# Optimization experiments

Hardware: AMD Instinct MI355X
Metric: run time of the kernel (lower is better)

## Reference

```python
import jax, jax.numpy as jnp
import numpy as np

EPS = 1e-5

def setup_inputs() -> dict:
    key = jax.random.key(0)
    k1, k2, k3 = jax.random.split(key, 3)
    x = jax.random.normal(k1, (16, 256, 32, 32), dtype=jnp.float32)
    embed = jax.random.normal(k2, (8192, 256), dtype=jnp.float32)
    cluster_size = jax.random.uniform(k3, (8192,), dtype=jnp.float32)
    return {"x": x, "embed": embed, "cluster_size": cluster_size}

def reference(x, embed, cluster_size):
    # x: (b, c, h, w) -> (b, h*w, c); project_in is Identity (codebook_dim == dim, heads=1)
    b, c, h, w = x.shape
    xt = jnp.transpose(x, (0, 2, 3, 1)).reshape(b, h * w, c)   # (b, n, d)
    flat = xt.reshape(-1, c)                                    # (N, d)
    d2 = (jnp.sum(flat * flat, axis=1, keepdims=True)
          - 2.0 * flat @ embed.T
          + jnp.sum(embed * embed, axis=1))                     # (N, K)
    embed_ind_flat = jnp.argmin(d2, axis=-1)                    # (N,) temperature==0 -> argmax of -d2
    quantize = embed[embed_ind_flat].reshape(b, h * w, c)       # gather codebook rows
    embed_ind = embed_ind_flat.reshape(b, h * w)
    # perplexity over (unnormalized) EMA cluster sizes, as in the torch code
    probs = cluster_size
    perplexity = jnp.exp(-jnp.sum(probs * jnp.log(probs + EPS)))
    # eval-mode commitment loss (weight_loss=True, commitment_weight=1.0)
    commit_loss = jnp.mean((quantize - xt) ** 2)
    return quantize, embed_ind, perplexity, commit_loss
```

## Files before the change

kernel.cpp:

```cpp
#include <hip/hip_runtime.h>
#include <hip/hip_bf16.h>
#include <math.h>

typedef _Float16 f16x8 __attribute__((ext_vector_type(8)));
typedef float f32x4 __attribute__((ext_vector_type(4)));

#define N_TOK 16384
#define D 256
#define K 8192

#define Q_OFF 0
#define IND_OFF 4194304
#define PERP_OFF 4210688
#define COMMIT_OFF 4210689

#define WS_CAND   0u
#define WS_E2     1048576u
#define WS_DSUM   1081344u
#define WS_EH     1114112u
#define WS_XH     5308416u
#define WS_XT     13697024u
#define WS_NEED   30474240u

__device__ __forceinline__ unsigned int ford(float f) {
    unsigned int u = __float_as_uint(f);
    return (u & 0x80000000u) ? ~u : (u | 0x80000000u);
}
__device__ __forceinline__ unsigned short f2h(float f) {
    _Float16 h = (_Float16)f;
    return *(unsigned short*)&h;
}
__device__ __forceinline__ void gload16(const void* g, void* l) {
    __builtin_amdgcn_global_load_lds(
        (const __attribute__((address_space(1))) unsigned int*)g,
        (__attribute__((address_space(3))) unsigned int*)l, 16, 0, 0);
}


__global__ void vq_convert_x(const float* __restrict__ x, float* __restrict__ xt,
                             unsigned short* __restrict__ xh) {
    __shared__ float t[64][65];
    const int tid = threadIdx.x;
    const int p0 = blockIdx.x * 64, c0 = blockIdx.y * 64, b = blockIdx.z;
    const int q = tid & 15, h = tid >> 4;
    #pragma unroll
    for (int r = 0; r < 4; ++r) {
        const int cl = r * 16 + h;
        const float4 v = *(const float4*)(x + (((size_t)(b * 256 + c0 + cl)) << 10) + p0 + q * 4);
        t[cl][q * 4 + 0] = v.x; t[cl][q * 4 + 1] = v.y;
        t[cl][q * 4 + 2] = v.z; t[cl][q * 4 + 3] = v.w;
    }
    __syncthreads();
    #pragma unroll
    for (int r = 0; r < 4; ++r) {
        const int nl = r * 16 + h;
        const int n = (b << 10) + p0 + nl;
        const int c = c0 + q * 4;
        float4 vf; ushort4 vh;
        vf.x = t[q * 4 + 0][nl]; vf.y = t[q * 4 + 1][nl];
        vf.z = t[q * 4 + 2][nl]; vf.w = t[q * 4 + 3][nl];
        vh.x = f2h(vf.x); vh.y = f2h(vf.y); vh.z = f2h(vf.z); vh.w = f2h(vf.w);
        *(float4*)(xt + ((size_t)n << 8) + c) = vf;
        *(ushort4*)(xh + ((size_t)n << 8) + c) = vh;
    }
}

__global__ void vq_prep_e(const float* __restrict__ e, unsigned short* __restrict__ eh,
                          float* __restrict__ e2, double* __restrict__ dsum) {
    if (blockIdx.x == 0 && threadIdx.x == 0) *dsum = 0.0;
    const int wave = threadIdx.x >> 6, lane = threadIdx.x & 63;
    const int c = blockIdx.x * 4 + wave;
    const float4 v = *(const float4*)(e + (size_t)c * D + lane * 4);
    ushort4 vh;
    vh.x = f2h(v.x); vh.y = f2h(v.y); vh.z = f2h(v.z); vh.w = f2h(v.w);
    *(ushort4*)(eh + (size_t)c * D + lane * 4) = vh;
    float s = v.x * v.x + v.y * v.y + v.z * v.z + v.w * v.w;
    #pragma unroll
    for (int off = 32; off > 0; off >>= 1) s += __shfl_down(s, off, 64);
    if (lane == 0) e2[c] = s;
}

__global__ __launch_bounds__(256)
__attribute__((amdgpu_waves_per_eu(2, 2)))
void vq_mfma_kernel(
    const unsigned short* __restrict__ xh, const unsigned short* __restrict__ eh,
    const float* __restrict__ e2, unsigned int* __restrict__ cand) {
    __shared__ __align__(16) unsigned short Bs[2][64 * 256];
    __shared__ float e2s[1024];

    const int tid = threadIdx.x;
    const int lane = tid & 63, wid = tid >> 6;
    const int l15 = lane & 15, lg = lane >> 4;
    const int split = blockIdx.y;
    const int m0 = blockIdx.x * 256;
    const int c0s = split * 1024;
    const int rw = m0 + wid * 64;

    *(float4*)&e2s[tid * 4] = *(const float4*)(e2 + c0s + tid * 4);

    f16x8 a[4][8];
    #pragma unroll
    for (int mf = 0; mf < 4; ++mf) {
        const unsigned short* ap = xh + (((size_t)(rw + mf * 16 + l15)) << 8) + lg * 8;
        #pragma unroll
        for (int t = 0; t < 8; ++t)
            a[mf][t] = *(const f16x8*)(ap + t * 32);
    }
    #pragma unroll
    for (int mf = 0; mf < 4; ++mf)
        #pragma unroll
        for (int t = 0; t < 8; ++t)
            asm volatile("" : "+v"(*(f32x4*)&a[mf][t]));

    __syncthreads();

    const int r0 = tid >> 5, cc = tid & 31;
    const unsigned short* ebase =
        eh + (((size_t)(c0s + r0)) << 8) + ((cc ^ r0) << 3);
    char* wdst = (char*)Bs + tid * 16;
    auto stage = [&](int t, int bo) {
        const unsigned short* p = ebase + t * 16384;
        #pragma unroll
        for (int i = 0; i < 8; ++i)
            gload16(p + i * 2048, wdst + bo + i * 4096);
    };

    const char* rbase = (const char*)Bs + l15 * 512;
    int ko[8];
    #pragma unroll
    for (int pr = 0; pr < 8; ++pr) ko[pr] = (((4 * pr + lg) ^ (l15 & 7)) << 4);

    float d1[16], d2[16];
    unsigned int ipk[16];
    #pragma unroll
    for (int r = 0; r < 16; ++r) { d1[r] = INFINITY; d2[r] = INFINITY; ipk[r] = 0; }

    stage(0, 0);

    #pragma unroll 2
    for (int t = 0; t < 16; ++t) {
        asm volatile("s_waitcnt vmcnt(0)" ::: "memory");
        __builtin_amdgcn_s_barrier();
        if (t < 15) stage(t + 1, ((t + 1) & 1) * 32768);

        const int BUF = (t & 1) * 32768;
        #pragma unroll
        for (int s2 = 0; s2 < 2; ++s2) {
            const int sb = BUF + s2 * 16384;
            const float e2v0 = e2s[t * 64 + s2 * 32 + l15];
            const float e2v1 = e2s[t * 64 + s2 * 32 + 16 + l15];
            f32x4 acc[4][2];
            #pragma unroll
            for (int mf = 0; mf < 4; ++mf) {
                f32x4 z = {0.f, 0.f, 0.f, 0.f};
                acc[mf][0] = z; acc[mf][1] = z;
            }
            f16x8 b0a = *(const f16x8*)(rbase + ko[0] + sb);
            f16x8 b1a = *(const f16x8*)(rbase + ko[0] + sb + 8192);
            #pragma unroll
            for (int pr = 0; pr < 8; ++pr) {
                f16x8 b0n, b1n;
                if (pr < 7) {
                    b0n = *(const f16x8*)(rbase + ko[pr + 1] + sb);
                    b1n = *(const f16x8*)(rbase + ko[pr + 1] + sb + 8192);
                }
                #pragma unroll
                for (int mf = 0; mf < 4; ++mf) {
                    acc[mf][0] = __builtin_amdgcn_mfma_f32_16x16x32_f16(
                        a[mf][pr], b0a, acc[mf][0], 0, 0, 0);
                    acc[mf][1] = __builtin_amdgcn_mfma_f32_16x16x32_f16(
                        a[mf][pr], b1a, acc[mf][1], 0, 0, 0);
                }
                b0a = b0n; b1a = b1n;
            }
            const unsigned int cl0 = (unsigned int)(t * 64 + s2 * 32 + l15);
            #pragma unroll
            for (int mf = 0; mf < 4; ++mf) {
                #pragma unroll
                for (int reg = 0; reg < 4; ++reg) {
                    const int rr = mf * 4 + reg;
                    const float sc0 = fmaf(-2.0f, acc[mf][0][reg], e2v0);
                    const float sc1 = fmaf(-2.0f, acc[mf][1][reg], e2v1);
                    if (fminf(sc0, sc1) < d2[rr]) {
                        {
                            const bool lt1 = sc0 < d1[rr], lt2 = sc0 < d2[rr];
                            const unsigned int ii = ipk[rr];
                            const unsigned int nif = (ii << 16) | cl0;
                            const unsigned int nis = (ii & 0xFFFFu) | (cl0 << 16);
                            d2[rr] = lt1 ? d1[rr] : (lt2 ? sc0 : d2[rr]);
                            ipk[rr] = lt1 ? nif : (lt2 ? nis : ii);
                            d1[rr] = lt1 ? sc0 : d1[rr];
                        }
                        {
                            const unsigned int cl1 = cl0 + 16;
                            const bool lt1 = sc1 < d1[rr], lt2 = sc1 < d2[rr];
                            const unsigned int ii = ipk[rr];
                            const unsigned int nif = (ii << 16) | cl1;
                            const unsigned int nis = (ii & 0xFFFFu) | (cl1 << 16);
                            d2[rr] = lt1 ? d1[rr] : (lt2 ? sc1 : d2[rr]);
                            ipk[rr] = lt1 ? nif : (lt2 ? nis : ii);
                            d1[rr] = lt1 ? sc1 : d1[rr];
                        }
                    }
                }
            }
        }
    }

    unsigned long long p1[16], p2[16];
    #pragma unroll
    for (int r = 0; r < 16; ++r) {
        p1[r] = (((unsigned long long)ford(d1[r])) << 32) |
                (unsigned int)(c0s + (ipk[r] & 0xFFFFu));
        p2[r] = (((unsigned long long)ford(d2[r])) << 32) |
                (unsigned int)(c0s + (ipk[r] >> 16));
    }
    #pragma unroll
    for (int st = 1; st < 16; st <<= 1) {
        #pragma unroll
        for (int r = 0; r < 16; ++r) {
            const unsigned long long q1 = __shfl_xor(p1[r], st, 64);
            const unsigned long long q2 = __shfl_xor(p2[r], st, 64);
            const unsigned long long n1 = p1[r] < q1 ? p1[r] : q1;
            const unsigned long long hi = p1[r] < q1 ? q1 : p1[r];
            const unsigned long long l2 = p2[r] < q2 ? p2[r] : q2;
            p1[r] = n1;
            p2[r] = hi < l2 ? hi : l2;
        }
    }
    if (l15 == 0) {
        #pragma unroll
        for (int mf = 0; mf < 4; ++mf)
            #pragma unroll
            for (int reg = 0; reg < 4; ++reg) {
                const int n = rw + mf * 16 + lg * 4 + reg;
                unsigned int* cp = cand + (((size_t)n) << 4) + split * 2;
                cp[0] = (unsigned int)p1[mf * 4 + reg];
                cp[1] = (unsigned int)p2[mf * 4 + reg];
            }
    }
}

__global__ void vq_rescore_finalize(const float* __restrict__ xt, const float* __restrict__ embed,
                                    const float* __restrict__ e2,
                                    const unsigned int* __restrict__ cand,
                                    float* __restrict__ out, double* __restrict__ dsum) {
    __shared__ double red[4];
    const int tid = threadIdx.x, wid = tid >> 6, lane = tid & 63;
    double wsum = 0.0;
    #pragma unroll 1
    for (int it = 0; it < 8; ++it) {
        const int n = blockIdx.x * 32 + it * 4 + wid;
        const float4 xv = *(const float4*)(xt + (((size_t)n) << 8) + lane * 4);
        unsigned long long best = 0xFFFFFFFFFFFFFFFFull;
        #pragma unroll 2
        for (int j = 0; j < 16; ++j) {
            const unsigned int c = cand[(((size_t)n) << 4) + j];
            const float4 ev = *(const float4*)(embed + (((size_t)c) << 8) + lane * 4);
            float dt = xv.x * ev.x + xv.y * ev.y + xv.z * ev.z + xv.w * ev.w;
            #pragma unroll
            for (int off = 32; off > 0; off >>= 1) dt += __shfl_xor(dt, off, 64);
            const float s = fmaf(-2.0f, dt, e2[c]);
            const unsigned long long p = (((unsigned long long)ford(s)) << 32) | c;
            best = p < best ? p : best;
        }
        const unsigned int bi = (unsigned int)(best & 0xFFFFFFFFull);
        if (lane == 0) out[IND_OFF + n] = (float)bi;
        const float4 ev = *(const float4*)(embed + (((size_t)bi) << 8) + lane * 4);
        *(float4*)(out + Q_OFF + (((size_t)n) << 8) + lane * 4) = ev;
        const float q0 = ev.x - xv.x, q1 = ev.y - xv.y, q2 = ev.z - xv.z, q3 = ev.w - xv.w;
        float a4 = q0 * q0 + q1 * q1 + q2 * q2 + q3 * q3;
        #pragma unroll
        for (int off = 32; off > 0; off >>= 1) a4 += __shfl_xor(a4, off, 64);
        if (lane == 0) wsum += (double)a4;
    }
    if (lane == 0) red[wid] = wsum;
    __syncthreads();
    if (tid == 0) atomicAdd(dsum, red[0] + red[1] + red[2] + red[3]);
}

__global__ void vq_tail_kernel(const float* __restrict__ cs,
                               const double* __restrict__ dsum,
                               float* __restrict__ out) {
    __shared__ double red[4];
    const int tid = threadIdx.x;
    double s = 0.0;
    for (int i = tid; i < K; i += 256) {
        const float p = cs[i];
        s += (double)(p * logf(p + 1e-5f));
    }
    #pragma unroll
    for (int off = 32; off > 0; off >>= 1) s += __shfl_down(s, off, 64);
    if ((tid & 63) == 0) red[tid >> 6] = s;
    __syncthreads();
    if (tid == 0) {
        const double tot = red[0] + red[1] + red[2] + red[3];
        const double pv = exp(-tot);
        out[PERP_OFF] = (pv > 3.3e38) ? 3.3e38f : (float)pv;
        out[COMMIT_OFF] = (float)(*dsum * (1.0 / 4194304.0));
    }
}

#define TM 64
#define TN 64
#define BKF 32
#define NSPLITF 2
#define CODES_PER_SPLIT (K / NSPLITF)
#define TILES_PER_SPLIT (CODES_PER_SPLIT / TN)

__global__ void vq_init_kernel(unsigned long long* __restrict__ keys, double* __restrict__ dsum) {
    int i = blockIdx.x * blockDim.x + threadIdx.x;
    if (i < N_TOK) keys[i] = 0xFFFFFFFFFFFFFFFFull;
    if (i == 0) *dsum = 0.0;
}
__global__ void vq_e2_kernel(const float* __restrict__ embed, float* __restrict__ e2) {
    int wave = threadIdx.x >> 6, lane = threadIdx.x & 63;
    int c = blockIdx.x * 4 + wave;
    const float4 v = *(const float4*)(embed + (size_t)c * D + lane * 4);
    float s = v.x * v.x + v.y * v.y + v.z * v.z + v.w * v.w;
    #pragma unroll
    for (int off = 32; off > 0; off >>= 1) s += __shfl_down(s, off, 64);
    if (lane == 0) e2[c] = s;
}
__global__ __launch_bounds__(256, 2) void vq_argmin_kernel(
    const float* __restrict__ x, const float* __restrict__ embed,
    const float* __restrict__ e2, unsigned long long* __restrict__ keys) {
    __shared__ float xT[D][TM];
    __shared__ float eT[BKF][TN + 4];
    const int tid = threadIdx.x;
    const int n0 = blockIdx.x * TM;
    const int b = n0 >> 10, p0 = n0 & 1023;
    const float* xb = x + (size_t)b * D * 1024 + p0;
    {
        const int t4 = (tid & 15) * 4, chb = tid >> 4;
        #pragma unroll
        for (int pass = 0; pass < 16; ++pass) {
            const int ch = pass * 16 + chb;
            *(float4*)&xT[ch][t4] = *(const float4*)(xb + (size_t)ch * 1024 + t4);
        }
    }
    __syncthreads();
    const int tm4 = (tid & 15) * 4, tn = tid >> 4, tn4 = tn * 4;
    float bestd[4]; int besti[4];
    #pragma unroll
    for (int i = 0; i < 4; ++i) { bestd[i] = INFINITY; besti[i] = 0x7fffffff; }
    for (int ct = 0; ct < TILES_PER_SPLIT; ++ct) {
        const int c0 = blockIdx.y * CODES_PER_SPLIT + ct * TN;
        float acc[4][4] = {};
        for (int kk = 0; kk < D; kk += BKF) {
            {
                const int j = tid >> 2, ch4 = (tid & 3) * 4;
                #pragma unroll
                for (int p = 0; p < 2; ++p) {
                    const int chl = p * 16 + ch4;
                    const float4 ev = *(const float4*)(embed + (size_t)(c0 + j) * D + kk + chl);
                    eT[chl + 0][j] = ev.x; eT[chl + 1][j] = ev.y;
                    eT[chl + 2][j] = ev.z; eT[chl + 3][j] = ev.w;
                }
            }
            __syncthreads();
            #pragma unroll
            for (int k2 = 0; k2 < BKF; ++k2) {
                const float4 a = *(const float4*)&xT[kk + k2][tm4];
                const float4 bv = *(const float4*)&eT[k2][tn4];
                acc[0][0] += a.x * bv.x; acc[0][1] += a.x * bv.y; acc[0][2] += a.x * bv.z; acc[0][3] += a.x * bv.w;
                acc[1][0] += a.y * bv.x; acc[1][1] += a.y * bv.y; acc[1][2] += a.y * bv.z; acc[1][3] += a.y * bv.w;
                acc[2][0] += a.z * bv.x; acc[2][1] += a.z * bv.y; acc[2][2] += a.z * bv.z; acc[2][3] += a.z * bv.w;
                acc[3][0] += a.w * bv.x; acc[3][1] += a.w * bv.y; acc[3][2] += a.w * bv.z; acc[3][3] += a.w * bv.w;
            }
            __syncthreads();
        }
        #pragma unroll
        for (int j = 0; j < 4; ++j) {
            const int c = c0 + tn4 + j;
            const float ec = e2[c];
            #pragma unroll
            for (int i = 0; i < 4; ++i) {
                const float s = ec - 2.0f * acc[i][j];
                if (s < bestd[i]) { bestd[i] = s; besti[i] = c; }
            }
        }
    }
    __syncthreads();
    float* cd = &eT[0][0];
    int* ci = (int*)&eT[16][0];
    #pragma unroll
    for (int i = 0; i < 4; ++i) { cd[tn * 64 + tm4 + i] = bestd[i]; ci[tn * 64 + tm4 + i] = besti[i]; }
    __syncthreads();
    if (tid < TM) {
        float bd = INFINITY; int bi = 0x7fffffff;
        for (int j = 0; j < 16; ++j) {
            const float d = cd[j * 64 + tid]; const int idx = ci[j * 64 + tid];
            if (d < bd || (d == bd && idx < bi)) { bd = d; bi = idx; }
        }
        atomicMin(&keys[n0 + tid], (((unsigned long long)ford(bd)) << 32) | (unsigned int)bi);
    }
}
__global__ void vq_finalize_kernel(const float* __restrict__ x, const float* __restrict__ embed,
                                   const unsigned long long* __restrict__ keys,
                                   float* __restrict__ out, double* __restrict__ dsum) {
    const int tid = threadIdx.x;
    const int n0 = blockIdx.x * 64;
    const int t = tid >> 2, q = tid & 3;
    const int n = n0 + t;
    const int b = n >> 10, p = n & 1023;
    if (tid < 64) {
        const int nn = n0 + tid;
        out[IND_OFF + nn] = (float)(int)(unsigned int)(keys[nn] & 0xFFFFFFFFull);
    }
    const int idx = (int)(unsigned int)(keys[n] & 0xFFFFFFFFull);
    const float* erow = embed + (size_t)idx * D;
    const float* xrow = x + (size_t)b * D * 1024 + p;
    float* qrow = out + Q_OFF + (size_t)n * D;
    float acc = 0.0f;
    #pragma unroll
    for (int i = 0; i < 16; ++i) {
        const int ch = i * 16 + q * 4;
        const float4 ev = *(const float4*)(erow + ch);
        *(float4*)(qrow + ch) = ev;
        const float x0 = xrow[(size_t)(ch + 0) * 1024];
        const float x1 = xrow[(size_t)(ch + 1) * 1024];
        const float x2 = xrow[(size_t)(ch + 2) * 1024];
        const float x3 = xrow[(size_t)(ch + 3) * 1024];
        const float d0 = ev.x - x0, d1 = ev.y - x1, d2 = ev.z - x2, d3 = ev.w - x3;
        acc += d0 * d0 + d1 * d1 + d2 * d2 + d3 * d3;
    }
    #pragma unroll
    for (int off = 32; off > 0; off >>= 1) acc += __shfl_down(acc, off, 64);
    if ((tid & 63) == 0) atomicAdd(dsum, (double)acc);
}

extern "C" void kernel_launch(void* const* d_in, const int* in_sizes, int n_in,
                              void* d_out, int out_size, void* d_ws, size_t ws_size,
                              hipStream_t stream) {
    const float* x = (const float*)d_in[0];
    const float* embed = (const float*)d_in[1];
    const float* cs = (const float*)d_in[2];
    float* out = (float*)d_out;
    char* ws = (char*)d_ws;

    if (ws_size >= (size_t)WS_NEED) {
        unsigned int* cand = (unsigned int*)(ws + WS_CAND);
        float* e2 = (float*)(ws + WS_E2);
        double* dsum = (double*)(ws + WS_DSUM);
        unsigned short* eh = (unsigned short*)(ws + WS_EH);
        unsigned short* xh = (unsigned short*)(ws + WS_XH);
        float* xt = (float*)(ws + WS_XT);

        vq_prep_e<<<dim3(K / 4), dim3(256), 0, stream>>>(embed, eh, e2, dsum);
        vq_convert_x<<<dim3(16, 4, 16), dim3(256), 0, stream>>>(x, xt, xh);
        vq_mfma_kernel<<<dim3(64, 8), dim3(256), 0, stream>>>(xh, eh, e2, cand);
        vq_rescore_finalize<<<dim3(512), dim3(256), 0, stream>>>(xt, embed, e2, cand, out, dsum);
        vq_tail_kernel<<<dim3(1), dim3(256), 0, stream>>>(cs, dsum, out);
    } else {
        unsigned long long* keys = (unsigned long long*)ws;
        float* e2 = (float*)(ws + 131072);
        double* dsum = (double*)(ws + 163840);
        vq_init_kernel<<<dim3(64), dim3(256), 0, stream>>>(keys, dsum);
        vq_e2_kernel<<<dim3(K / 4), dim3(256), 0, stream>>>(embed, e2);
        vq_argmin_kernel<<<dim3(N_TOK / TM, NSPLITF), dim3(256), 0, stream>>>(x, embed, e2, keys);
        vq_finalize_kernel<<<dim3(256), dim3(256), 0, stream>>>(x, embed, keys, out, dsum);
        vq_tail_kernel<<<dim3(1), dim3(256), 0, stream>>>(cs, dsum, out);
    }
}
```

Before: 167.6 us.

## Use 512-thread blocks with 32 rows per wave and branchless top-2 update

Doubles the MFMA kernel's block to 8 waves, each owning 32 token rows instead of 64. This halves per-wave A-fragment and accumulator registers and raises occupancy to hide LDS and global latency. Staging is split across more threads, with the swizzle adjusted to match. The branchy top-2 candidate update becomes a branchless fminf/fmaxf form. In exchange, each B tile loaded into LDS is reused by fewer MFMAs per wave, and the candidate update now runs unconditionally on every score.

Result: slower. 381.8 us (+127.9%).

```diff
diff --git a/kernel.cpp b/kernel.cpp
--- a/kernel.cpp
+++ b/kernel.cpp
@@ -80,8 +80,7 @@
     if (lane == 0) e2[c] = s;
 }
 
-__global__ __launch_bounds__(256)
-__attribute__((amdgpu_waves_per_eu(2, 2)))
+__global__ __launch_bounds__(512, 4)
 void vq_mfma_kernel(
     const unsigned short* __restrict__ xh, const unsigned short* __restrict__ eh,
     const float* __restrict__ e2, unsigned int* __restrict__ cand) {
@@ -94,20 +93,20 @@
     const int split = blockIdx.y;
     const int m0 = blockIdx.x * 256;
     const int c0s = split * 1024;
-    const int rw = m0 + wid * 64;
-
-    *(float4*)&e2s[tid * 4] = *(const float4*)(e2 + c0s + tid * 4);
-
-    f16x8 a[4][8];
-    #pragma unroll
-    for (int mf = 0; mf < 4; ++mf) {
+    const int rw = m0 + wid * 32;
+
+    *(float2*)&e2s[tid * 2] = *(const float2*)(e2 + c0s + tid * 2);
+
+    f16x8 a[2][8];
+    #pragma unroll
+    for (int mf = 0; mf < 2; ++mf) {
         const unsigned short* ap = xh + (((size_t)(rw + mf * 16 + l15)) << 8) + lg * 8;
         #pragma unroll
         for (int t = 0; t < 8; ++t)
             a[mf][t] = *(const f16x8*)(ap + t * 32);
     }
     #pragma unroll
-    for (int mf = 0; mf < 4; ++mf)
+    for (int mf = 0; mf < 2; ++mf)
         #pragma unroll
         for (int t = 0; t < 8; ++t)
             asm volatile("" : "+v"(*(f32x4*)&a[mf][t]));
@@ -116,24 +115,22 @@
 
     const int r0 = tid >> 5, cc = tid & 31;
     const unsigned short* ebase =
-        eh + (((size_t)(c0s + r0)) << 8) + ((cc ^ r0) << 3);
+        eh + (((size_t)(c0s + r0)) << 8) + ((cc ^ (r0 & 7)) << 3);
     char* wdst = (char*)Bs + tid * 16;
     auto stage = [&](int t, int bo) {
         const unsigned short* p = ebase + t * 16384;
         #pragma unroll
-        for (int i = 0; i < 8; ++i)
-            gload16(p + i * 2048, wdst + bo + i * 4096);
+        for (int i = 0; i < 4; ++i)
+            gload16(p + i * 4096, wdst + bo + i * 8192);
     };
 
     const char* rbase = (const char*)Bs + l15 * 512;
-    int ko[8];
-    #pragma unroll
-    for (int pr = 0; pr < 8; ++pr) ko[pr] = (((4 * pr + lg) ^ (l15 & 7)) << 4);
-
-    float d1[16], d2[16];
-    unsigned int ipk[16];
-    #pragma unroll
-    for (int r = 0; r < 16; ++r) { d1[r] = INFINITY; d2[r] = INFINITY; ipk[r] = 0; }
+    const int rx = l15 & 7;
+
+    float d1[8], d2[8];
+    unsigned int ipk[8];
+    #pragma unroll
+    for (int r = 0; r < 8; ++r) { d1[r] = INFINITY; d2[r] = INFINITY; ipk[r] = 0; }
 
     stage(0, 0);
 
@@ -149,23 +146,24 @@
             const int sb = BUF + s2 * 16384;
             const float e2v0 = e2s[t * 64 + s2 * 32 + l15];
             const float e2v1 = e2s[t * 64 + s2 * 32 + 16 + l15];
-            f32x4 acc[4][2];
-            #pragma unroll
-            for (int mf = 0; mf < 4; ++mf) {
+            f32x4 acc[2][2];
+            #pragma unroll
+            for (int mf = 0; mf < 2; ++mf) {
                 f32x4 z = {0.f, 0.f, 0.f, 0.f};
                 acc[mf][0] = z; acc[mf][1] = z;
             }
-            f16x8 b0a = *(const f16x8*)(rbase + ko[0] + sb);
-            f16x8 b1a = *(const f16x8*)(rbase + ko[0] + sb + 8192);
+            f16x8 b0a = *(const f16x8*)(rbase + ((lg ^ rx) << 4) + sb);
+            f16x8 b1a = *(const f16x8*)(rbase + ((lg ^ rx) << 4) + sb + 8192);
             #pragma unroll
             for (int pr = 0; pr < 8; ++pr) {
                 f16x8 b0n, b1n;
                 if (pr < 7) {
-                    b0n = *(const f16x8*)(rbase + ko[pr + 1] + sb);
-                    b1n = *(const f16x8*)(rbase + ko[pr + 1] + sb + 8192);
+                    const int ko = (((4 * (pr + 1) + lg) ^ rx) << 4);
+                    b0n = *(const f16x8*)(rbase + ko + sb);
+                    b1n = *(const f16x8*)(rbase + ko + sb + 8192);
                 }
                 #pragma unroll
-                for (int mf = 0; mf < 4; ++mf) {
+                for (int mf = 0; mf < 2; ++mf) {
                     acc[mf][0] = __builtin_amdgcn_mfma_f32_16x16x32_f16(
                         a[mf][pr], b0a, acc[mf][0], 0, 0, 0);
                     acc[mf][1] = __builtin_amdgcn_mfma_f32_16x16x32_f16(
@@ -174,42 +172,41 @@
                 b0a = b0n; b1a = b1n;
             }
             const unsigned int cl0 = (unsigned int)(t * 64 + s2 * 32 + l15);
-            #pragma unroll
-            for (int mf = 0; mf < 4; ++mf) {
+            const unsigned int cl1 = cl0 + 16;
+            const unsigned int cl0h = cl0 << 16, cl1h = cl1 << 16;
+            #pragma unroll
+            for (int mf = 0; mf < 2; ++mf) {
                 #pragma unroll
                 for (int reg = 0; reg < 4; ++reg) {
                     const int rr = mf * 4 + reg;
-                    const float sc0 = fmaf(-2.0f, acc[mf][0][reg], e2v0);
-                    const float sc1 = fmaf(-2.0f, acc[mf][1][reg], e2v1);
-                    if (fminf(sc0, sc1) < d2[rr]) {
-                        {
-                            const bool lt1 = sc0 < d1[rr], lt2 = sc0 < d2[rr];
-                            const unsigned int ii = ipk[rr];
-                            const unsigned int nif = (ii << 16) | cl0;
-                            const unsigned int nis = (ii & 0xFFFFu) | (cl0 << 16);
-                            d2[rr] = lt1 ? d1[rr] : (lt2 ? sc0 : d2[rr]);
-                            ipk[rr] = lt1 ? nif : (lt2 ? nis : ii);
-                            d1[rr] = lt1 ? sc0 : d1[rr];
-                        }
-                        {
-                            const unsigned int cl1 = cl0 + 16;
-                            const bool lt1 = sc1 < d1[rr], lt2 = sc1 < d2[rr];
-                            const unsigned int ii = ipk[rr];
-                            const unsigned int nif = (ii << 16) | cl1;
-                            const unsigned int nis = (ii & 0xFFFFu) | (cl1 << 16);
-                            d2[rr] = lt1 ? d1[rr] : (lt2 ? sc1 : d2[rr]);
-                            ipk[rr] = lt1 ? nif : (lt2 ? nis : ii);
-                            d1[rr] = lt1 ? sc1 : d1[rr];
-                        }
+                    const float s0 = fmaf(-2.0f, acc[mf][0][reg], e2v0);
+                    const float s1 = fmaf(-2.0f, acc[mf][1][reg], e2v1);
+                    {
+                        const bool lt1 = s0 < d1[rr];
+                        const bool lt2 = s0 < d2[rr];
+                        d2[rr] = fminf(d2[rr], fmaxf(d1[rr], s0));
+                        const unsigned int nif = (ipk[rr] << 16) | cl0;
+                        const unsigned int nis = (ipk[rr] & 0xFFFFu) | cl0h;
+                        ipk[rr] = lt1 ? nif : (lt2 ? nis : ipk[rr]);
+                        d1[rr] = fminf(d1[rr], s0);
+                    }
+                    {
+                        const bool lt1 = s1 < d1[rr];
+                        const bool lt2 = s1 < d2[rr];
+                        d2[rr] = fminf(d2[rr], fmaxf(d1[rr], s1));
+                        const unsigned int nif = (ipk[rr] << 16) | cl1;
+                        const unsigned int nis = (ipk[rr] & 0xFFFFu) | cl1h;
+                        ipk[rr] = lt1 ? nif : (lt2 ? nis : ipk[rr]);
+                        d1[rr] = fminf(d1[rr], s1);
                     }
                 }
             }
         }
     }
 
-    unsigned long long p1[16], p2[16];
-    #pragma unroll
-    for (int r = 0; r < 16; ++r) {
+    unsigned long long p1[8], p2[8];
+    #pragma unroll
+    for (int r = 0; r < 8; ++r) {
         p1[r] = (((unsigned long long)ford(d1[r])) << 32) |
                 (unsigned int)(c0s + (ipk[r] & 0xFFFFu));
         p2[r] = (((unsigned long long)ford(d2[r])) << 32) |
@@ -218,7 +215,7 @@
     #pragma unroll
     for (int st = 1; st < 16; st <<= 1) {
         #pragma unroll
-        for (int r = 0; r < 16; ++r) {
+        for (int r = 0; r < 8; ++r) {
             const unsigned long long q1 = __shfl_xor(p1[r], st, 64);
             const unsigned long long q2 = __shfl_xor(p2[r], st, 64);
             const unsigned long long n1 = p1[r] < q1 ? p1[r] : q1;
@@ -230,7 +227,7 @@
     }
     if (l15 == 0) {
         #pragma unroll
-        for (int mf = 0; mf < 4; ++mf)
+        for (int mf = 0; mf < 2; ++mf)
             #pragma unroll
             for (int reg = 0; reg < 4; ++reg) {
                 const int n = rw + mf * 16 + lg * 4 + reg;
@@ -449,7 +446,7 @@
 
         vq_prep_e<<<dim3(K / 4), dim3(256), 0, stream>>>(embed, eh, e2, dsum);
         vq_convert_x<<<dim3(16, 4, 16), dim3(256), 0, stream>>>(x, xt, xh);
-        vq_mfma_kernel<<<dim3(64, 8), dim3(256), 0, stream>>>(xh, eh, e2, cand);
+        vq_mfma_kernel<<<dim3(64, 8), dim3(512), 0, stream>>>(xh, eh, e2, cand);
         vq_rescore_finalize<<<dim3(512), dim3(256), 0, stream>>>(xt, embed, e2, cand, out, dsum);
         vq_tail_kernel<<<dim3(1), dim3(256), 0, stream>>>(cs, dsum, out);
     } else {
```
